# Performance work log

Hardware: AMD Instinct MI355X
Metric: run time of the kernel (lower is better)

## Reference

```python
import jax, jax.numpy as jnp
import numpy as np

L, B, T, C, H, DF, V = 6, 8, 1024, 768, 12, 3072, 512
HD = C // H  # head_dim = 64
STD = 0.02
EPS = 1e-5


def layernorm(x, g, b):
    mu = jnp.mean(x, axis=-1, keepdims=True)
    var = jnp.mean(jnp.square(x - mu), axis=-1, keepdims=True)
    return (x - mu) * jax.lax.rsqrt(var + EPS) * g + b


def setup_inputs() -> dict:
    key = jax.random.key(0)
    ks = jax.random.split(key, 8)
    # weights stored as [in, out] so forward is x @ W (== torch x @ W.T)
    tok_emb = jax.random.normal(ks[0], (V, C), jnp.float32) * STD
    pos_emb = jax.random.normal(ks[1], (T, C), jnp.float32) * STD
    Wqkv = jax.random.normal(ks[2], (L, C, 3 * C), jnp.float32) * STD
    Wproj = jax.random.normal(ks[3], (L, C, C), jnp.float32) * STD
    W1 = jax.random.normal(ks[4], (L, C, DF), jnp.float32) * STD
    b1 = jnp.zeros((L, DF), jnp.float32)
    W2 = jax.random.normal(ks[5], (L, DF, C), jnp.float32) * STD
    b2 = jnp.zeros((L, C), jnp.float32)
    ln1_g = jnp.ones((L, C), jnp.float32); ln1_b = jnp.zeros((L, C), jnp.float32)
    ln2_g = jnp.ones((L, C), jnp.float32); ln2_b = jnp.zeros((L, C), jnp.float32)
    lnf_g = jnp.ones((C,), jnp.float32); lnf_b = jnp.zeros((C,), jnp.float32)
    idx = jax.random.randint(ks[6], (B, T), 0, V, jnp.int64 if jax.config.jax_enable_x64 else jnp.int32)
    return {"idx": idx, "tok_emb": tok_emb, "pos_emb": pos_emb, "Wqkv": Wqkv,
            "Wproj": Wproj, "W1": W1, "b1": b1, "W2": W2, "b2": b2,
            "ln1_g": ln1_g, "ln1_b": ln1_b, "ln2_g": ln2_g, "ln2_b": ln2_b,
            "lnf_g": lnf_g, "lnf_b": lnf_b}


def reference(idx, tok_emb, pos_emb, Wqkv, Wproj, W1, b1, W2, b2,
              ln1_g, ln1_b, ln2_g, ln2_b, lnf_g, lnf_b):
    Bx, Tx = idx.shape
    x = tok_emb[idx] + pos_emb[:Tx][None, :, :]  # [B,T,C]
    causal = jnp.triu(jnp.ones((Tx, Tx), bool), k=1)  # True above diagonal
    scale = np.sqrt(HD).astype(np.float32)
    neg_inf = jnp.asarray(-jnp.inf, x.dtype)
    for l in range(L):
        # --- causal self-attention ---
        xn = layernorm(x, ln1_g[l], ln1_b[l])
        qkv = jnp.einsum('btc,cd->btd', xn, Wqkv[l])  # [B,T,3C]
        q, k, v = jnp.split(qkv, 3, axis=-1)
        q = q.reshape(Bx, Tx, H, HD)
        k = k.reshape(Bx, Tx, H, HD)
        v = v.reshape(Bx, Tx, H, HD)
        scores = jnp.einsum('bthd,bshd->bhts', q, k) / scale  # [B,H,T,T]
        scores = jnp.where(causal, neg_inf, scores)
        w = jax.nn.softmax(scores, axis=-1)
        attn = jnp.einsum('bhts,bshd->bthd', w, v).reshape(Bx, Tx, C)
        x = x + jnp.einsum('btc,cd->btd', attn, Wproj[l])
        # --- MLP ---
        xn = layernorm(x, ln2_g[l], ln2_b[l])
        h = jax.nn.gelu(jnp.einsum('btc,cf->btf', xn, W1[l]) + b1[l], approximate=False)
        x = x + jnp.einsum('btf,fc->btc', h, W2[l]) + b2[l]
    logits = jnp.einsum('btc,vc->btv', layernorm(x, lnf_g, lnf_b), tok_emb)  # tied head
    return logits
```

## Files before the change

### kernel.cpp

```cpp
#include <hip/hip_runtime.h>
#include <hip/hip_bf16.h>
#include <stdint.h>

#define LNUM 6
#define BB 8
#define TT 1024
#define CC 768
#define HH 12
#define HDIM 64
#define DFF 3072
#define VV 512
#define MM (BB*TT)
#define QKREG ((size_t)BB*HH*TT*64)

typedef __bf16 bf16x8 __attribute__((ext_vector_type(8)));
typedef float f32x4 __attribute__((ext_vector_type(4)));

__device__ __forceinline__ uint16_t f2b(float f) {
  uint32_t u = __float_as_uint(f);
  u += 0x7FFFu + ((u >> 16) & 1u);
  return (uint16_t)(u >> 16);
}

__device__ __forceinline__ float b2f(uint16_t u) {
  return __uint_as_float((uint32_t)u << 16);
}

__device__ __forceinline__ void gld16(const uint16_t* g, uint16_t* l) {
  __builtin_amdgcn_global_load_lds(
      (const __attribute__((address_space(1))) uint32_t*)g,
      (__attribute__((address_space(3))) uint32_t*)l, 16, 0, 0);
}

__device__ __forceinline__ f32x4 mfma16(bf16x8 a, bf16x8 b, f32x4 c) {
  return __builtin_amdgcn_mfma_f32_16x16x32_bf16(a, b, c, 0, 0, 0);
}

__global__ __launch_bounds__(256) void cvt4_k(const float* __restrict__ in,
                                              uint16_t* __restrict__ out, int n4) {
  const int gid = blockIdx.x * 256 + threadIdx.x;
  if (gid >= n4) return;
  const float4 v = ((const float4*)in)[gid];
  ushort4 w; w.x = f2b(v.x); w.y = f2b(v.y); w.z = f2b(v.z); w.w = f2b(v.w);
  ((ushort4*)out)[gid] = w;
}

__global__ __launch_bounds__(256) void embed_k(const int* __restrict__ idx,
                                               const float* __restrict__ tok,
                                               const float* __restrict__ pos,
                                               float* __restrict__ x) {
  const int gid = blockIdx.x * 256 + threadIdx.x;
  const int row = gid / (CC / 4), c4 = gid % (CC / 4);
  const int t = row & (TT - 1);
  const int tkn = idx[row];
  const float4 a = ((const float4*)(tok + (size_t)tkn * CC))[c4];
  const float4 q = ((const float4*)(pos + (size_t)t * CC))[c4];
  ((float4*)(x + (size_t)row * CC))[c4] =
      make_float4(a.x + q.x, a.y + q.y, a.z + q.z, a.w + q.w);
}

__global__ __launch_bounds__(256) void ln_k(const float* __restrict__ x,
                                            const float* __restrict__ gamma,
                                            const float* __restrict__ beta,
                                            uint16_t* __restrict__ o) {
  const int lane = threadIdx.x & 63, wid = threadIdx.x >> 6;
  const int row = blockIdx.x * 4 + wid;
  const float4* xr = (const float4*)(x + (size_t)row * CC);
  float4 v[3]; float s = 0.f, sq = 0.f;
#pragma unroll
  for (int i = 0; i < 3; ++i) {
    v[i] = xr[lane + i * 64];
    s += v[i].x + v[i].y + v[i].z + v[i].w;
    sq += v[i].x * v[i].x + v[i].y * v[i].y + v[i].z * v[i].z + v[i].w * v[i].w;
  }
#pragma unroll
  for (int m = 1; m < 64; m <<= 1) { s += __shfl_xor(s, m, 64); sq += __shfl_xor(sq, m, 64); }
  const float mu = s * (1.f / 768.f);
  const float rstd = rsqrtf(sq * (1.f / 768.f) - mu * mu + 1e-5f);
  ushort4* orow = (ushort4*)(o + (size_t)row * CC);
#pragma unroll
  for (int i = 0; i < 3; ++i) {
    const int c4 = lane + i * 64;
    const float4 gg = ((const float4*)gamma)[c4];
    const float4 bb = ((const float4*)beta)[c4];
    ushort4 w;
    w.x = f2b((v[i].x - mu) * rstd * gg.x + bb.x);
    w.y = f2b((v[i].y - mu) * rstd * gg.y + bb.y);
    w.z = f2b((v[i].z - mu) * rstd * gg.z + bb.z);
    w.w = f2b((v[i].w - mu) * rstd * gg.w + bb.w);
    orow[c4] = w;
  }
}

template <int NP>
__global__ __launch_bounds__(256) void lnrb_k(float* __restrict__ x,
                                              const uint16_t* __restrict__ pp,
                                              const float* __restrict__ gamma,
                                              const float* __restrict__ beta,
                                              uint16_t* __restrict__ o) {
  const int lane = threadIdx.x & 63, wid = threadIdx.x >> 6;
  const int row = blockIdx.x * 4 + wid;
  float4* xr = (float4*)(x + (size_t)row * CC);
  float4 v[3]; float s = 0.f, sq = 0.f;
#pragma unroll
  for (int i = 0; i < 3; ++i) {
    const int c4 = lane + i * 64;
    float4 a = xr[c4];
#pragma unroll
    for (int j = 0; j < NP; ++j) {
      const ushort4 q =
          ((const ushort4*)(pp + (size_t)j * MM * CC + (size_t)row * CC))[c4];
      a.x += b2f(q.x); a.y += b2f(q.y); a.z += b2f(q.z); a.w += b2f(q.w);
    }
    xr[c4] = a;
    v[i] = a;
    s += a.x + a.y + a.z + a.w;
    sq += a.x * a.x + a.y * a.y + a.z * a.z + a.w * a.w;
  }
#pragma unroll
  for (int m = 1; m < 64; m <<= 1) { s += __shfl_xor(s, m, 64); sq += __shfl_xor(sq, m, 64); }
  const float mu = s * (1.f / 768.f);
  const float rstd = rsqrtf(sq * (1.f / 768.f) - mu * mu + 1e-5f);
  ushort4* orow = (ushort4*)(o + (size_t)row * CC);
#pragma unroll
  for (int i = 0; i < 3; ++i) {
    const int c4 = lane + i * 64;
    const float4 gg = ((const float4*)gamma)[c4];
    const float4 bb = ((const float4*)beta)[c4];
    ushort4 w;
    w.x = f2b((v[i].x - mu) * rstd * gg.x + bb.x);
    w.y = f2b((v[i].y - mu) * rstd * gg.y + bb.y);
    w.z = f2b((v[i].z - mu) * rstd * gg.z + bb.z);
    w.w = f2b((v[i].w - mu) * rstd * gg.w + bb.w);
    orow[c4] = w;
  }
}

__global__ __launch_bounds__(256) void tca_k(const float* __restrict__ Wq,
                                             const float* __restrict__ Wp,
                                             const float* __restrict__ W1p,
                                             const float* __restrict__ W2p,
                                             uint16_t* __restrict__ dq,
                                             uint16_t* __restrict__ dp,
                                             uint16_t* __restrict__ d1,
                                             uint16_t* __restrict__ d2) {
  __shared__ float tile[32][33];
  const int b = blockIdx.x;
  const int l = b / 6912;
  int r = b - l * 6912;
  const float* src; uint16_t* dst; int K, N, kt, nt;
  if (r < 1728) {
    K = CC; N = 3 * CC;
    src = Wq + (size_t)l * CC * 3 * CC; dst = dq + (size_t)l * CC * 3 * CC;
    kt = r / 72; nt = r % 72;
  } else if (r < 2304) {
    r -= 1728; K = CC; N = CC;
    src = Wp + (size_t)l * CC * CC; dst = dp + (size_t)l * CC * CC;
    kt = r / 24; nt = r % 24;
  } else if (r < 4608) {
    r -= 2304; K = CC; N = DFF;
    src = W1p + (size_t)l * CC * DFF; dst = d1 + (size_t)l * CC * DFF;
    kt = r / 96; nt = r % 96;
  } else {
    r -= 4608; K = DFF; N = CC;
    src = W2p + (size_t)l * DFF * CC; dst = d2 + (size_t)l * DFF * CC;
    kt = r / 24; nt = r % 24;
  }
  const int tx = threadIdx.x & 31, ty = threadIdx.x >> 5;
  const int kb = kt * 32, nb = nt * 32;
#pragma unroll
  for (int i = 0; i < 32; i += 8)
    tile[ty + i][tx] = src[(size_t)(kb + ty + i) * N + nb + tx];
  __syncthreads();
#pragma unroll
  for (int i = 0; i < 32; i += 8)
    dst[(size_t)(nb + ty + i) * K + kb + tx] = f2b(tile[tx][ty + i]);
}

template <int EPI>
__global__ __launch_bounds__(256) void gemm_k(const uint16_t* __restrict__ A,
                                              const uint16_t* __restrict__ Bt,
                                              int N, int K,
                                              const float* __restrict__ bias,
                                              uint16_t* __restrict__ outb,
                                              float* __restrict__ outf) {
  __shared__ __align__(16) uint16_t As[128 * 64];
  __shared__ __align__(16) uint16_t Bs[128 * 64];
  const int tid = threadIdx.x;
  const int lane = tid & 63, wid = tid >> 6;
  const int wm = wid >> 1, wn = wid & 1;
  const int bm = blockIdx.x * 128, bn = blockIdx.y * 128;
  const int kp = blockIdx.z;
  const int Ksub = K / (int)gridDim.z;
  const int k0b = kp * Ksub;
  const int nkt = Ksub >> 6;
  const int srow = tid >> 3;
  const int swz = (tid & 7) ^ (srow & 7);
  const uint16_t* gA0 = A + (size_t)(bm + srow) * K + k0b + swz * 8;
  const uint16_t* gB0 = Bt + (size_t)(bn + srow) * K + k0b + swz * 8;
  const size_t qs = (size_t)32 * K;
  const int l15 = lane & 15, lhi = lane >> 4;
  int aof[2][4], bof[2][4];
#pragma unroll
  for (int kk = 0; kk < 2; ++kk)
#pragma unroll
    for (int i = 0; i < 4; ++i) {
      const int sw = ((kk * 4 + lhi) ^ (l15 & 7)) * 16;
      aof[kk][i] = (wm * 64 + i * 16 + l15) * 128 + sw;
      bof[kk][i] = (wn * 64 + i * 16 + l15) * 128 + sw;
    }
  f32x4 acc[4][4] = {};
  for (int t = 0; t < nkt; ++t) {
    const int ko = t * 64;
#pragma unroll
    for (int q = 0; q < 4; ++q) {
      gld16(gA0 + q * qs + ko, &As[q * 2048 + tid * 8]);
      gld16(gB0 + q * qs + ko, &Bs[q * 2048 + tid * 8]);
    }
    __syncthreads();
    const char* Ab = (const char*)As;
    const char* Bb = (const char*)Bs;
#pragma unroll
    for (int kk = 0; kk < 2; ++kk) {
      bf16x8 a[4], b[4];
#pragma unroll
      for (int i = 0; i < 4; ++i) {
        a[i] = *(const bf16x8*)(Ab + aof[kk][i]);
        b[i] = *(const bf16x8*)(Bb + bof[kk][i]);
      }
#pragma unroll
      for (int i = 0; i < 4; ++i)
#pragma unroll
        for (int j = 0; j < 4; ++j)
          acc[i][j] = mfma16(a[i], b[j], acc[i][j]);
    }
    __syncthreads();
  }
#pragma unroll
  for (int i = 0; i < 4; ++i) {
    const int m0 = bm + wm * 64 + i * 16 + (lhi << 2);
#pragma unroll
    for (int j = 0; j < 4; ++j) {
      const int n = bn + wn * 64 + j * 16 + l15;
      if constexpr (EPI == 5) {
        const int sec = n / CC;
        const int rn = n - sec * CC;
        const int hh = rn >> 6, d = rn & 63;
        const int b = m0 >> 10, t0 = m0 & 1023;
        if (sec == 2) {
          ushort4 w;
          w.x = f2b(acc[i][j][0]); w.y = f2b(acc[i][j][1]);
          w.z = f2b(acc[i][j][2]); w.w = f2b(acc[i][j][3]);
          *(ushort4*)(outb + 2 * QKREG + ((size_t)(b * HH + hh) * 64 + d) * TT + t0) = w;
        } else {
          uint16_t* dst = outb + (size_t)sec * QKREG + ((size_t)(b * HH + hh) * TT + t0) * 64 + d;
#pragma unroll
          for (int rr = 0; rr < 4; ++rr) dst[(size_t)rr * 64] = f2b(acc[i][j][rr]);
        }
      } else if constexpr (EPI == 8) {
        uint16_t* pdst = outb + (size_t)kp * ((size_t)MM * N);
        const float bb = (kp == 0 && bias) ? bias[n] : 0.f;
#pragma unroll
        for (int rr = 0; rr < 4; ++rr)
          pdst[(size_t)(m0 + rr) * N + n] = f2b(acc[i][j][rr] + bb);
      } else {
#pragma unroll
        for (int rr = 0; rr < 4; ++rr) {
          const size_t o = (size_t)(m0 + rr) * N + n;
          const float v = acc[i][j][rr];
          if constexpr (EPI == 1) {
            outf[o] = v;
          } else if constexpr (EPI == 2) {
            float t = v + bias[n];
            t = 0.5f * t * (1.0f + erff(t * 0.70710678118654752f));
            outb[o] = f2b(t);
          }
        }
      }
    }
  }
}

__global__ __launch_bounds__(256) void attn_k(const uint16_t* __restrict__ qkvh,
                                              uint16_t* __restrict__ ao) {
  __shared__ __align__(16) uint16_t Ks[64 * 64], Vs[64 * 64];
  __shared__ __align__(16) uint16_t Ps[4][16 * 64];
  const int tid = threadIdx.x, lane = tid & 63, wid = tid >> 6;
  const int qt = (TT / 64 - 1) - blockIdx.x / (BB * HH);
  const int bh = blockIdx.x % (BB * HH);
  const uint16_t* qb = qkvh + (size_t)bh * (TT * 64);
  const uint16_t* kb = qkvh + QKREG + (size_t)bh * (TT * 64);
  const uint16_t* vb = qkvh + 2 * QKREG + (size_t)bh * ((size_t)64 * TT);
  const int l15 = lane & 15, lhi = lane >> 4;
  bf16x8 qf[2];
  {
    const uint16_t* qr = qb + (size_t)(qt * 64 + wid * 16 + l15) * 64 + lhi * 8;
    qf[0] = *(const bf16x8*)qr;
    qf[1] = *(const bf16x8*)(qr + 32);
  }
  const int c0 = tid, c1 = tid + 256;
  const int r0 = c0 >> 3, r1 = c1 >> 3;
  const int cb0 = (c0 & 7) * 16, cb1 = (c1 & 7) * 16;
  const int ph0 = r0 * 128 + (cb0 ^ ((r0 & 7) << 4));
  const int ph1 = r1 * 128 + (cb1 ^ ((r1 & 7) << 4));

  uint4 kr0, kr1, vr0, vr1;
  kr0 = *(const uint4*)(kb + (size_t)r0 * 64 + cb0 / 2);
  kr1 = *(const uint4*)(kb + (size_t)r1 * 64 + cb1 / 2);
  vr0 = *(const uint4*)(vb + (size_t)r0 * TT + cb0 / 2);
  vr1 = *(const uint4*)(vb + (size_t)r1 * TT + cb1 / 2);
  *(uint4*)((char*)Ks + ph0) = kr0;
  *(uint4*)((char*)Ks + ph1) = kr1;
  *(uint4*)((char*)Vs + ph0) = vr0;
  *(uint4*)((char*)Vs + ph1) = vr1;
  __syncthreads();

  f32x4 oacc[4] = {};
  float mrun[4] = {-INFINITY, -INFINITY, -INFINITY, -INFINITY};
  float lrun[4] = {0.f, 0.f, 0.f, 0.f};
  char* pb = (char*)Ps[wid];

  for (int j = 0; j <= qt; ++j) {
    const bool more = (j < qt);
    if (more) {
      const int jn = (j + 1) * 64;
      kr0 = *(const uint4*)(kb + (size_t)(jn + r0) * 64 + cb0 / 2);
      kr1 = *(const uint4*)(kb + (size_t)(jn + r1) * 64 + cb1 / 2);
      vr0 = *(const uint4*)(vb + (size_t)r0 * TT + jn + cb0 / 2);
      vr1 = *(const uint4*)(vb + (size_t)r1 * TT + jn + cb1 / 2);
    }
    f32x4 s4[4] = {};
    __builtin_amdgcn_s_setprio(1);
#pragma unroll
    for (int kk = 0; kk < 2; ++kk) {
      const int cbyte = kk * 64 + lhi * 16;
#pragma unroll
      for (int nt = 0; nt < 4; ++nt) {
        const int krow = nt * 16 + l15;
        const bf16x8 kf = *(const bf16x8*)((char*)Ks + krow * 128 + (cbyte ^ ((krow & 7) << 4)));
        s4[nt] = mfma16(qf[kk], kf, s4[nt]);
      }
    }
    __builtin_amdgcn_s_setprio(0);
    const bool diag = (j == qt);
    float alpha[4];
#pragma unroll
    for (int r = 0; r < 4; ++r) {
      const int qg = qt * 64 + wid * 16 + (lhi << 2) + r;
      float mx = -INFINITY;
#pragma unroll
      for (int nt = 0; nt < 4; ++nt) {
        float v = s4[nt][r] * 0.125f;
        if (diag && (j * 64 + nt * 16 + l15) > qg) v = -INFINITY;
        s4[nt][r] = v;
        mx = fmaxf(mx, v);
      }
#pragma unroll
      for (int m = 1; m < 16; m <<= 1) mx = fmaxf(mx, __shfl_xor(mx, m, 16));
      const float mnew = fmaxf(mrun[r], mx);
      alpha[r] = __expf(mrun[r] - mnew);
      float ps = 0.f;
#pragma unroll
      for (int nt = 0; nt < 4; ++nt) {
        const float pp = __expf(s4[nt][r] - mnew);
        s4[nt][r] = pp;
        ps += pp;
      }
#pragma unroll
      for (int m = 1; m < 16; m <<= 1) ps += __shfl_xor(ps, m, 16);
      lrun[r] = lrun[r] * alpha[r] + ps;
      mrun[r] = mnew;
    }
#pragma unroll
    for (int dt = 0; dt < 4; ++dt)
#pragma unroll
      for (int r = 0; r < 4; ++r) oacc[dt][r] *= alpha[r];
#pragma unroll
    for (int r = 0; r < 4; ++r) {
      const int prow = (lhi << 2) + r;
      const int swp = (prow & 7) << 4;
#pragma unroll
      for (int nt = 0; nt < 4; ++nt) {
        const int cb = (nt * 16 + l15) * 2;
        *(uint16_t*)(pb + prow * 128 + (cb ^ swp)) = f2b(s4[nt][r]);
      }
    }
    __builtin_amdgcn_s_setprio(1);
#pragma unroll
    for (int kk = 0; kk < 2; ++kk) {
      const int cbyte = kk * 64 + lhi * 16;
      const bf16x8 pf = *(const bf16x8*)(pb + l15 * 128 + (cbyte ^ ((l15 & 7) << 4)));
#pragma unroll
      for (int dt = 0; dt < 4; ++dt) {
        const int vrow = dt * 16 + l15;
        const bf16x8 vf = *(const bf16x8*)((char*)Vs + vrow * 128 + (cbyte ^ ((vrow & 7) << 4)));
        oacc[dt] = mfma16(pf, vf, oacc[dt]);
      }
    }
    __builtin_amdgcn_s_setprio(0);
    __syncthreads();
    if (more) {
      *(uint4*)((char*)Ks + ph0) = kr0;
      *(uint4*)((char*)Ks + ph1) = kr1;
      *(uint4*)((char*)Vs + ph0) = vr0;
      *(uint4*)((char*)Vs + ph1) = vr1;
    }
    __syncthreads();
  }
#pragma unroll
  for (int dt = 0; dt < 4; ++dt) {
#pragma unroll
    for (int r = 0; r < 4; ++r) {
      const int q = qt * 64 + wid * 16 + (lhi << 2) + r;
      const float v = oacc[dt][r] / lrun[r];
      ao[(size_t)((bh / HH) * TT + q) * CC + (bh % HH) * HDIM + dt * 16 + l15] = f2b(v);
    }
  }
}

extern "C" void kernel_launch(void* const* d_in, const int* in_sizes, int n_in,
                              void* d_out, int out_size, void* d_ws, size_t ws_size,
                              hipStream_t stream) {
  (void)in_sizes; (void)n_in; (void)out_size;
  const int*   idx  = (const int*)d_in[0];
  const float* tok  = (const float*)d_in[1];
  const float* pos  = (const float*)d_in[2];
  const float* Wqkv = (const float*)d_in[3];
  const float* Wpro = (const float*)d_in[4];
  const float* W1   = (const float*)d_in[5];
  const float* b1   = (const float*)d_in[6];
  const float* W2   = (const float*)d_in[7];
  const float* b2   = (const float*)d_in[8];
  const float* g1   = (const float*)d_in[9];
  const float* be1  = (const float*)d_in[10];
  const float* g2   = (const float*)d_in[11];
  const float* be2  = (const float*)d_in[12];
  const float* gf   = (const float*)d_in[13];
  const float* bfb  = (const float*)d_in[14];
  float* out = (float*)d_out;

  const size_t QS = (size_t)CC * 3 * CC;
  const size_t PS = (size_t)CC * CC;
  const size_t S1 = (size_t)CC * DFF;
  const size_t S2 = (size_t)DFF * CC;

  char* p = (char*)d_ws;
  float* x = (float*)p;            p += (size_t)MM * CC * 4;
  uint16_t* act = (uint16_t*)p;    p += (size_t)MM * CC * 2;
  uint16_t* big = (uint16_t*)p;    p += (size_t)MM * DFF * 2;
  uint16_t* tokb = (uint16_t*)p;   p += (size_t)VV * CC * 2;
  uint16_t* partb = (uint16_t*)p;  p += (size_t)2 * MM * CC * 2;
  char* pbase = p;
  uint16_t* wqA = (uint16_t*)p;    p += QS * LNUM * 2;
  uint16_t* wpA = (uint16_t*)p;    p += PS * LNUM * 2;
  uint16_t* w1A = (uint16_t*)p;    p += S1 * LNUM * 2;
  uint16_t* w2A = (uint16_t*)p;    p += S2 * LNUM * 2;
  const bool roomy2 = ws_size >= (size_t)(p - (char*)d_ws);
  if (!roomy2) {
    p = pbase;
    wqA = (uint16_t*)p; p += QS * 2;
    wpA = (uint16_t*)p; p += PS * 2;
    w1A = (uint16_t*)p; p += S1 * 2;
    w2A = (uint16_t*)p; p += S2 * 2;
  }

  cvt4_k<<<dim3((VV * CC / 4 + 255) / 256), 256, 0, stream>>>(tok, tokb, VV * CC / 4);
  embed_k<<<dim3(MM * (CC / 4) / 256), 256, 0, stream>>>(idx, tok, pos, x);
  ln_k<<<dim3(MM / 4), 256, 0, stream>>>(x, g1, be1, act);
  if (roomy2)
    tca_k<<<dim3(LNUM * 6912), 256, 0, stream>>>(Wqkv, Wpro, W1, W2, wqA, wpA, w1A, w2A);

  for (int l = 0; l < LNUM; ++l) {
    if (!roomy2)
      tca_k<<<dim3(6912), 256, 0, stream>>>(Wqkv + (size_t)l * QS, Wpro + (size_t)l * PS,
                                            W1 + (size_t)l * S1, W2 + (size_t)l * S2,
                                            wqA, wpA, w1A, w2A);
    const size_t lw = roomy2 ? (size_t)l : 0;
    gemm_k<5><<<dim3(MM / 128, 3 * CC / 128, 1), 256, 0, stream>>>(
        act, wqA + lw * QS, 3 * CC, CC, nullptr, big, nullptr);
    attn_k<<<dim3((TT / 64) * BB * HH), 256, 0, stream>>>(big, act);
    gemm_k<8><<<dim3(MM / 128, CC / 128, 2), 256, 0, stream>>>(
        act, wpA + lw * PS, CC, CC, nullptr, partb, nullptr);
    lnrb_k<2><<<dim3(MM / 4), 256, 0, stream>>>(x, partb,
                                                g2 + (size_t)l * CC, be2 + (size_t)l * CC, act);
    gemm_k<2><<<dim3(MM / 128, DFF / 128, 1), 256, 0, stream>>>(
        act, w1A + lw * S1, DFF, CC, b1 + (size_t)l * DFF, big, nullptr);
    const float* ng = (l + 1 < LNUM) ? g1 + (size_t)(l + 1) * CC : gf;
    const float* nb = (l + 1 < LNUM) ? be1 + (size_t)(l + 1) * CC : bfb;
    gemm_k<8><<<dim3(MM / 128, CC / 128, 2), 256, 0, stream>>>(
        big, w2A + lw * S2, CC, DFF, b2 + (size_t)l * CC, partb, nullptr);
    lnrb_k<2><<<dim3(MM / 4), 256, 0, stream>>>(x, partb, ng, nb, act);
  }
  gemm_k<1><<<dim3(MM / 128, VV / 128, 1), 256, 0, stream>>>(
      act, tokb, VV, CC, nullptr, nullptr, out);
}
```

Measured before the change: 1.532 ms.

## Store residual stream in bf16 and double-buffer K/V tiles in attention

The fp32 residual stream x becomes bf16. Embedding, layernorm and residual-add kernels now read and write half the bytes, with the accumulation still done in fp32 registers. Separately, the attention kernel double-buffers its K/V shared-memory tiles, which cuts the per-iteration barriers from two to one. Keeping the residual in bf16 loses precision, and rounding error builds up over the six layers, so accuracy may drift.

Result: faster. 1.463 ms (-4.5%).

```diff
diff --git a/kernel.cpp b/kernel.cpp
--- a/kernel.cpp
+++ b/kernel.cpp
@@ -48,28 +48,31 @@
 __global__ __launch_bounds__(256) void embed_k(const int* __restrict__ idx,
                                                const float* __restrict__ tok,
                                                const float* __restrict__ pos,
-                                               float* __restrict__ x) {
+                                               uint16_t* __restrict__ x) {
   const int gid = blockIdx.x * 256 + threadIdx.x;
   const int row = gid / (CC / 4), c4 = gid % (CC / 4);
   const int t = row & (TT - 1);
   const int tkn = idx[row];
   const float4 a = ((const float4*)(tok + (size_t)tkn * CC))[c4];
   const float4 q = ((const float4*)(pos + (size_t)t * CC))[c4];
-  ((float4*)(x + (size_t)row * CC))[c4] =
-      make_float4(a.x + q.x, a.y + q.y, a.z + q.z, a.w + q.w);
-}
-
-__global__ __launch_bounds__(256) void ln_k(const float* __restrict__ x,
+  ushort4 w;
+  w.x = f2b(a.x + q.x); w.y = f2b(a.y + q.y);
+  w.z = f2b(a.z + q.z); w.w = f2b(a.w + q.w);
+  ((ushort4*)(x + (size_t)row * CC))[c4] = w;
+}
+
+__global__ __launch_bounds__(256) void ln_k(const uint16_t* __restrict__ x,
                                             const float* __restrict__ gamma,
                                             const float* __restrict__ beta,
                                             uint16_t* __restrict__ o) {
   const int lane = threadIdx.x & 63, wid = threadIdx.x >> 6;
   const int row = blockIdx.x * 4 + wid;
-  const float4* xr = (const float4*)(x + (size_t)row * CC);
+  const ushort4* xr = (const ushort4*)(x + (size_t)row * CC);
   float4 v[3]; float s = 0.f, sq = 0.f;
 #pragma unroll
   for (int i = 0; i < 3; ++i) {
-    v[i] = xr[lane + i * 64];
+    const ushort4 u = xr[lane + i * 64];
+    v[i] = make_float4(b2f(u.x), b2f(u.y), b2f(u.z), b2f(u.w));
     s += v[i].x + v[i].y + v[i].z + v[i].w;
     sq += v[i].x * v[i].x + v[i].y * v[i].y + v[i].z * v[i].z + v[i].w * v[i].w;
   }
@@ -93,26 +96,29 @@
 }
 
 template <int NP>
-__global__ __launch_bounds__(256) void lnrb_k(float* __restrict__ x,
+__global__ __launch_bounds__(256) void lnrb_k(uint16_t* __restrict__ x,
                                               const uint16_t* __restrict__ pp,
                                               const float* __restrict__ gamma,
                                               const float* __restrict__ beta,
                                               uint16_t* __restrict__ o) {
   const int lane = threadIdx.x & 63, wid = threadIdx.x >> 6;
   const int row = blockIdx.x * 4 + wid;
-  float4* xr = (float4*)(x + (size_t)row * CC);
+  ushort4* xr = (ushort4*)(x + (size_t)row * CC);
   float4 v[3]; float s = 0.f, sq = 0.f;
 #pragma unroll
   for (int i = 0; i < 3; ++i) {
     const int c4 = lane + i * 64;
-    float4 a = xr[c4];
+    const ushort4 u = xr[c4];
+    float4 a = make_float4(b2f(u.x), b2f(u.y), b2f(u.z), b2f(u.w));
 #pragma unroll
     for (int j = 0; j < NP; ++j) {
       const ushort4 q =
           ((const ushort4*)(pp + (size_t)j * MM * CC + (size_t)row * CC))[c4];
       a.x += b2f(q.x); a.y += b2f(q.y); a.z += b2f(q.z); a.w += b2f(q.w);
     }
-    xr[c4] = a;
+    ushort4 w;
+    w.x = f2b(a.x); w.y = f2b(a.y); w.z = f2b(a.z); w.w = f2b(a.w);
+    xr[c4] = w;
     v[i] = a;
     s += a.x + a.y + a.z + a.w;
     sq += a.x * a.x + a.y * a.y + a.z * a.z + a.w * a.w;
@@ -283,7 +289,7 @@
 
 __global__ __launch_bounds__(256) void attn_k(const uint16_t* __restrict__ qkvh,
                                               uint16_t* __restrict__ ao) {
-  __shared__ __align__(16) uint16_t Ks[64 * 64], Vs[64 * 64];
+  __shared__ __align__(16) uint16_t Ks[2][64 * 64], Vs[2][64 * 64];
   __shared__ __align__(16) uint16_t Ps[4][16 * 64];
   const int tid = threadIdx.x, lane = tid & 63, wid = tid >> 6;
   const int qt = (TT / 64 - 1) - blockIdx.x / (BB * HH);
@@ -309,11 +315,10 @@
   kr1 = *(const uint4*)(kb + (size_t)r1 * 64 + cb1 / 2);
   vr0 = *(const uint4*)(vb + (size_t)r0 * TT + cb0 / 2);
   vr1 = *(const uint4*)(vb + (size_t)r1 * TT + cb1 / 2);
-  *(uint4*)((char*)Ks + ph0) = kr0;
-  *(uint4*)((char*)Ks + ph1) = kr1;
-  *(uint4*)((char*)Vs + ph0) = vr0;
-  *(uint4*)((char*)Vs + ph1) = vr1;
-  __syncthreads();
+  *(uint4*)((char*)Ks[0] + ph0) = kr0;
+  *(uint4*)((char*)Ks[0] + ph1) = kr1;
+  *(uint4*)((char*)Vs[0] + ph0) = vr0;
+  *(uint4*)((char*)Vs[0] + ph1) = vr1;
 
   f32x4 oacc[4] = {};
   float mrun[4] = {-INFINITY, -INFINITY, -INFINITY, -INFINITY};
@@ -321,7 +326,9 @@
   char* pb = (char*)Ps[wid];
 
   for (int j = 0; j <= qt; ++j) {
+    const int cur = j & 1;
     const bool more = (j < qt);
+    __syncthreads();
     if (more) {
       const int jn = (j + 1) * 64;
       kr0 = *(const uint4*)(kb + (size_t)(jn + r0) * 64 + cb0 / 2);
@@ -329,6 +336,8 @@
       vr0 = *(const uint4*)(vb + (size_t)r0 * TT + jn + cb0 / 2);
       vr1 = *(const uint4*)(vb + (size_t)r1 * TT + jn + cb1 / 2);
     }
+    const char* Kb = (const char*)Ks[cur];
+    const char* Vb = (const char*)Vs[cur];
     f32x4 s4[4] = {};
     __builtin_amdgcn_s_setprio(1);
 #pragma unroll
@@ -337,7 +346,7 @@
 #pragma unroll
       for (int nt = 0; nt < 4; ++nt) {
         const int krow = nt * 16 + l15;
-        const bf16x8 kf = *(const bf16x8*)((char*)Ks + krow * 128 + (cbyte ^ ((krow & 7) << 4)));
+        const bf16x8 kf = *(const bf16x8*)(Kb + krow * 128 + (cbyte ^ ((krow & 7) << 4)));
         s4[nt] = mfma16(qf[kk], kf, s4[nt]);
       }
     }
@@ -393,19 +402,19 @@
 #pragma unroll
       for (int dt = 0; dt < 4; ++dt) {
         const int vrow = dt * 16 + l15;
-        const bf16x8 vf = *(const bf16x8*)((char*)Vs + vrow * 128 + (cbyte ^ ((vrow & 7) << 4)));
+        const bf16x8 vf = *(const bf16x8*)(Vb + vrow * 128 + (cbyte ^ ((vrow & 7) << 4)));
         oacc[dt] = mfma16(pf, vf, oacc[dt]);
       }
     }
     __builtin_amdgcn_s_setprio(0);
-    __syncthreads();
     if (more) {
-      *(uint4*)((char*)Ks + ph0) = kr0;
-      *(uint4*)((char*)Ks + ph1) = kr1;
-      *(uint4*)((char*)Vs + ph0) = vr0;
-      *(uint4*)((char*)Vs + ph1) = vr1;
-    }
-    __syncthreads();
+      char* kn = (char*)Ks[cur ^ 1];
+      char* vn = (char*)Vs[cur ^ 1];
+      *(uint4*)(kn + ph0) = kr0;
+      *(uint4*)(kn + ph1) = kr1;
+      *(uint4*)(vn + ph0) = vr0;
+      *(uint4*)(vn + ph1) = vr1;
+    }
   }
 #pragma unroll
   for (int dt = 0; dt < 4; ++dt) {
@@ -445,7 +454,7 @@
   const size_t S2 = (size_t)DFF * CC;
 
   char* p = (char*)d_ws;
-  float* x = (float*)p;            p += (size_t)MM * CC * 4;
+  uint16_t* x = (uint16_t*)p;      p += (size_t)MM * CC * 2;
   uint16_t* act = (uint16_t*)p;    p += (size_t)MM * CC * 2;
   uint16_t* big = (uint16_t*)p;    p += (size_t)MM * DFF * 2;
   uint16_t* tokb = (uint16_t*)p;   p += (size_t)VV * CC * 2;
```
